# Kernel tuning notes

Measured on AMD Instinct MI355X. Metric: run time of the kernel, lower is better.

Reference implementation:

```python
import jax, jax.numpy as jnp
import numpy as np

D_MODEL, D_HEAD, D_MLP, N_HEADS = 768, 64, 3072, 12
BATCH, SEQ = 1, 4096
LN_EPS = 1e-05
IGNORE = -100000.0


def setup_inputs() -> dict:
    key = jax.random.key(0)
    ks = jax.random.split(key, 8)
    s = 0.02
    return {
        "resid_pre": jax.random.normal(ks[0], (BATCH, SEQ, D_MODEL), jnp.float32),
        "ln1_w": jnp.ones((D_MODEL,), jnp.float32),
        "ln1_b": jnp.zeros((D_MODEL,), jnp.float32),
        "ln2_w": jnp.ones((D_MODEL,), jnp.float32),
        "ln2_b": jnp.zeros((D_MODEL,), jnp.float32),
        "W_Q": jax.random.normal(ks[1], (N_HEADS, D_MODEL, D_HEAD), jnp.float32) * s,
        "W_K": jax.random.normal(ks[2], (N_HEADS, D_MODEL, D_HEAD), jnp.float32) * s,
        "W_V": jax.random.normal(ks[3], (N_HEADS, D_MODEL, D_HEAD), jnp.float32) * s,
        "W_O": jax.random.normal(ks[4], (N_HEADS, D_HEAD, D_MODEL), jnp.float32) * s,
        "b_Q": jnp.zeros((N_HEADS, D_HEAD), jnp.float32),
        "b_K": jnp.zeros((N_HEADS, D_HEAD), jnp.float32),
        "b_V": jnp.zeros((N_HEADS, D_HEAD), jnp.float32),
        "b_O": jnp.zeros((D_MODEL,), jnp.float32),
        "W_in": jax.random.normal(ks[5], (D_MODEL, D_MLP), jnp.float32) * s,
        "b_in": jnp.zeros((D_MLP,), jnp.float32),
        "W_out": jax.random.normal(ks[6], (D_MLP, D_MODEL), jnp.float32) * s,
        "b_out": jnp.zeros((D_MODEL,), jnp.float32),
    }


def _layernorm(x, w, b):
    mean = jnp.mean(x, axis=-1, keepdims=True)
    var = jnp.var(x, axis=-1, keepdims=True)  # unbiased=False
    return (x - mean) * jax.lax.rsqrt(var + LN_EPS) * w + b


def _attention(x, W_Q, W_K, W_V, W_O, b_Q, b_K, b_V, b_O):
    # x: [b, s, d_model]; W_{Q,K,V}: [h, d_model, d_head]
    q = jnp.einsum("bsm,hmd->bshd", x, W_Q) + b_Q
    k = jnp.einsum("bsm,hmd->bshd", x, W_K) + b_K
    v = jnp.einsum("bsm,hmd->bshd", x, W_V) + b_V
    scores = jnp.einsum("bqhd,bkhd->bhqk", q, k) / np.sqrt(D_HEAD).astype(np.float32)
    seq = x.shape[1]
    causal = jnp.tril(jnp.ones((seq, seq), bool))  # True where allowed
    scores = jnp.where(causal, scores, IGNORE)
    pattern = jax.nn.softmax(scores, axis=-1)
    z = jnp.einsum("bkhd,bhqk->bqhd", v, pattern)
    return jnp.einsum("bqhd,hdm->bqm", z, W_O) + b_O


def reference(resid_pre, ln1_w, ln1_b, ln2_w, ln2_b,
              W_Q, W_K, W_V, W_O, b_Q, b_K, b_V, b_O,
              W_in, b_in, W_out, b_out):
    resid_mid = _attention(_layernorm(resid_pre, ln1_w, ln1_b),
                           W_Q, W_K, W_V, W_O, b_Q, b_K, b_V, b_O) + resid_pre
    pre = jnp.einsum("bsm,mf->bsf", _layernorm(resid_mid, ln2_w, ln2_b), W_in) + b_in
    post = jax.nn.gelu(pre, approximate=False)  # torch F.gelu default = exact erf
    mlp_out = jnp.einsum("bsf,fm->bsm", post, W_out) + b_out
    resid_post = mlp_out + resid_mid
    return (resid_post, post)
```

## Files before the change

kernel.cpp:

```cpp
#include <hip/hip_runtime.h>
#include <hip/hip_bf16.h>
#include <math.h>

using bf16 = __hip_bfloat16;
using u16  = unsigned short;
using u32  = unsigned int;
using short8 = __attribute__((ext_vector_type(8))) short;
using f32x4  = __attribute__((ext_vector_type(4))) float;

#define AS1 __attribute__((address_space(1)))
#define AS3 __attribute__((address_space(3)))

__device__ __forceinline__ void gld_lds16(const void* g, void* l) {
  __builtin_amdgcn_global_load_lds((const AS1 u32*)g, (AS3 u32*)l, 16, 0, 0);
}

__device__ __forceinline__ bool probe_f32(const void* p) {
  return *(const u32*)p == 0x3F800000u;
}
__device__ __forceinline__ float ldf(const void* p, size_t i, bool f32) {
  return f32 ? ((const float*)p)[i] : __bfloat162float(((const bf16*)p)[i]);
}
__device__ __forceinline__ void stf(void* p, size_t i, float v, bool f32) {
  if (f32) ((float*)p)[i] = v;
  else     ((bf16*)p)[i] = __float2bfloat16(v);
}
__device__ __forceinline__ u32 cvt_pk_bf16(float lo, float hi) {
  u32 r;
  asm("v_cvt_pk_bf16_f32 %0, %1, %2" : "=v"(r) : "v"(lo), "v"(hi));
  return r;
}

__global__ __launch_bounds__(256) void ln_kernel(const void* __restrict__ x,
    const void* __restrict__ w, const void* __restrict__ b, bf16* __restrict__ out,
    const void* probe, int x_is_f32)
{
  const bool pf = probe_f32(probe);
  const bool xf = x_is_f32 ? true : pf;
  const int row = blockIdx.x, t = threadIdx.x;
  const size_t base = (size_t)row * 768;
  float v[3]; float s1 = 0.f, s2 = 0.f;
#pragma unroll
  for (int i = 0; i < 3; ++i) { float f = ldf(x, base + i*256 + t, xf); v[i] = f; s1 += f; s2 += f*f; }
#pragma unroll
  for (int off = 32; off >= 1; off >>= 1) { s1 += __shfl_xor(s1, off); s2 += __shfl_xor(s2, off); }
  __shared__ float a1[4], a2[4];
  if ((t & 63) == 0) { a1[t>>6] = s1; a2[t>>6] = s2; }
  __syncthreads();
  float S1 = a1[0]+a1[1]+a1[2]+a1[3];
  float S2 = a2[0]+a2[1]+a2[2]+a2[3];
  float mean = S1 * (1.f/768.f);
  float var  = S2 * (1.f/768.f) - mean*mean;
  float rs = rsqrtf(var + 1e-5f);
#pragma unroll
  for (int i = 0; i < 3; ++i) {
    int c = i*256 + t;
    out[base + c] = __float2bfloat16((v[i]-mean)*rs*ldf(w, c, pf) + ldf(b, c, pf));
  }
}

__global__ __launch_bounds__(256) void prep_all(
    const void* W_Q, const void* W_K, const void* W_V, const void* Wo,
    const void* Win, const void* Wout,
    const void* bQ, const void* bK, const void* bV, const void* bO,
    const void* bIn, const void* bOut,
    bf16* __restrict__ qkvT, bf16* __restrict__ WoT, bf16* __restrict__ WinT,
    bf16* __restrict__ WoutT, float* __restrict__ biasA,
    const void* __restrict__ xres, const void* lw, const void* lb,
    bf16* __restrict__ lnout, const void* probe)
{
  const bool pf = probe_f32(probe);
  const int bid = blockIdx.x;
  const int t = threadIdx.x;
  if (bid >= 6939) {
    const int row = bid - 6939;
    const size_t base = (size_t)row * 768;
    float v[3]; float s1 = 0.f, s2 = 0.f;
#pragma unroll
    for (int i = 0; i < 3; ++i) { float f = ldf(xres, base + i*256 + t, pf); v[i] = f; s1 += f; s2 += f*f; }
#pragma unroll
    for (int off = 32; off >= 1; off >>= 1) { s1 += __shfl_xor(s1, off); s2 += __shfl_xor(s2, off); }
    __shared__ float a1[4], a2[4];
    if ((t & 63) == 0) { a1[t>>6] = s1; a2[t>>6] = s2; }
    __syncthreads();
    float S1 = a1[0]+a1[1]+a1[2]+a1[3];
    float S2 = a2[0]+a2[1]+a2[2]+a2[3];
    float mean = S1 * (1.f/768.f);
    float var  = S2 * (1.f/768.f) - mean*mean;
    float rs = rsqrtf(var + 1e-5f);
#pragma unroll
    for (int i = 0; i < 3; ++i) {
      int c = i*256 + t;
      lnout[base + c] = __float2bfloat16((v[i]-mean)*rs*ldf(lw, c, pf) + ldf(lb, c, pf));
    }
    return;
  }
  if (bid >= 6912) {
    int i = (bid - 6912)*256 + t;
    float v;
    if (i < 2304)      v = (i < 768) ? ldf(bQ, i, pf) : (i < 1536 ? ldf(bK, i-768, pf) : ldf(bV, i-1536, pf));
    else if (i < 3072) v = ldf(bO, i-2304, pf);
    else if (i < 6144) v = ldf(bIn, i-3072, pf);
    else               v = ldf(bOut, i-6144, pf);
    biasA[i] = v;
    return;
  }
  const void* src; bf16* dst; int R, C, bx, by; size_t soff = 0;
  if (bid < 1728) {
    int mtx = bid / 576, within = bid % 576;
    int h = within / 48, tt = within % 48;
    by = tt >> 1; bx = tt & 1;
    src = (mtx == 0) ? W_Q : (mtx == 1 ? W_K : W_V);
    soff = (size_t)h * 49152;
    dst = qkvT + ((size_t)mtx*768 + h*64) * 768;
    R = 768; C = 64;
  } else if (bid < 2304) {
    int within = bid - 1728; bx = within % 24; by = within / 24;
    src = Wo; dst = WoT; R = 768; C = 768;
  } else if (bid < 4608) {
    int within = bid - 2304; bx = within % 96; by = within / 96;
    src = Win; dst = WinT; R = 768; C = 3072;
  } else {
    int within = bid - 4608; bx = within % 24; by = within / 24;
    src = Wout; dst = WoutT; R = 3072; C = 768;
  }
  __shared__ bf16 tile[32][33];
  const int bc = bx*32, br = by*32;
  const int tx = t & 31, ty = t >> 5;
#pragma unroll
  for (int i = 0; i < 32; i += 8)
    tile[ty+i][tx] = __float2bfloat16(ldf(src, soff + (size_t)(br+ty+i)*C + bc + tx, pf));
  __syncthreads();
#pragma unroll
  for (int i = 0; i < 32; i += 8)
    dst[(size_t)(bc+ty+i)*R + br + tx] = tile[tx][ty+i];
}

template<int MODE, int BM, int BN, int BK>
__global__ __launch_bounds__(256) void gemm_bt(const bf16* __restrict__ A,
    const bf16* __restrict__ BT, const float* __restrict__ bias,
    const void* __restrict__ res, void* __restrict__ Cout, bf16* __restrict__ aux,
    size_t outOff, const void* probe, int M, int N, int K,
    float* __restrict__ zf, float* __restrict__ sf)
{
  constexpr int MR = BM/32, NR = BN/32;
  constexpr int CH = BK/8;
  __shared__ bf16 Alds[2][BM*BK];
  __shared__ bf16 Blds[2][BN*BK];
  const int tid = threadIdx.x;
  const int lane = tid & 63, w = tid >> 6;
  const int l15 = lane & 15, l4 = lane >> 4;

  const int nwg = gridDim.x * gridDim.y;
  const int L = blockIdx.x + blockIdx.y * gridDim.x;
  const int wid = (L & 7) * (nwg >> 3) + (L >> 3);
  const int bx = wid % gridDim.x, by = wid / gridDim.x;

  if (MODE == 0) {
    float4 z4 = {0.f, 0.f, 0.f, 0.f};
    float4* zp = (float4*)zf + (size_t)wid*1024;
#pragma unroll
    for (int i = 0; i < 4; ++i) zp[i*256 + tid] = z4;
    if (tid < 16) ((float4*)sf)[wid*16 + tid] = z4;
  }

  const int brow = by * BM, bcol = bx * BN;
  const int wr = (w >> 1) * (BM/2), wc = (w & 1) * (BN/2);
  const bf16* Ag = A  + (size_t)brow * K;
  const bf16* Bg = BT + (size_t)bcol * K;
  f32x4 acc[MR][NR];
#pragma unroll
  for (int i = 0; i < MR; ++i)
#pragma unroll
    for (int j = 0; j < NR; ++j) acc[i][j] = 0.f;

  auto swzf = [](int r) { return BK == 64 ? ((r ^ (r >> 3)) & 7) : ((r >> 1) & 3); };

  auto STAGE = [&](int bb, int kt) {
    if (MODE == 4) {
      const float* Zfp = (const float*)A;
      const float* sfh = sf + (size_t)(kt >> 6) * 4096 + brow;
#pragma unroll
      for (int i = 0; i < BM*CH/256; ++i) {
        int id = i*256 + tid, r = id >> 3, cc = id & 7;
        int sw = swzf(r);
        const float* srcp = Zfp + (size_t)(brow + r)*768 + kt + cc*8;
        float4 f0 = *(const float4*)srcp;
        float4 f1 = *(const float4*)(srcp + 4);
        float sc = __builtin_amdgcn_rcpf(sfh[r]);
        u32 pk[4];
        pk[0] = cvt_pk_bf16(f0.x*sc, f0.y*sc);
        pk[1] = cvt_pk_bf16(f0.z*sc, f0.w*sc);
        pk[2] = cvt_pk_bf16(f1.x*sc, f1.y*sc);
        pk[3] = cvt_pk_bf16(f1.z*sc, f1.w*sc);
        *(uint4*)((char*)Alds[bb] + r*(BK*2) + ((cc ^ sw) << 4)) = *(uint4*)pk;
      }
    } else {
#pragma unroll
      for (int i = 0; i < (BM*CH + 255)/256; ++i) {
        int id = i*256 + tid;
        if ((BM*CH % 256) == 0 || id < BM*CH) {
          int r = id / CH, cc = id % CH;
          gld_lds16(Ag + (size_t)r*K + kt + ((cc ^ swzf(r)) * 8), (char*)Alds[bb] + id*16);
        }
      }
    }
#pragma unroll
    for (int i = 0; i < (BN*CH + 255)/256; ++i) {
      int id = i*256 + tid;
      if ((BN*CH % 256) == 0 || id < BN*CH) {
        int r = id / CH, cc = id % CH;
        gld_lds16(Bg + (size_t)r*K + kt + ((cc ^ swzf(r)) * 8), (char*)Blds[bb] + id*16);
      }
    }
  };

  STAGE(0, 0);
  __syncthreads();

  const int nIt = K / BK;
  for (int it = 0; it < nIt; ++it) {
    const int cur = it & 1;
    if (it + 1 < nIt) STAGE(cur ^ 1, (it + 1) * BK);
#pragma unroll
    for (int kk = 0; kk < BK/32; ++kk) {
      short8 a[MR], b[NR];
#pragma unroll
      for (int mi = 0; mi < MR; ++mi) {
        int row = wr + mi*16 + l15;
        a[mi] = *(const short8*)((const char*)Alds[cur] + row*(BK*2) + (((kk*4 + l4) ^ swzf(row)) << 4));
      }
#pragma unroll
      for (int ni = 0; ni < NR; ++ni) {
        int row = wc + ni*16 + l15;
        b[ni] = *(const short8*)((const char*)Blds[cur] + row*(BK*2) + (((kk*4 + l4) ^ swzf(row)) << 4));
      }
      __builtin_amdgcn_s_setprio(1);
#pragma unroll
      for (int mi = 0; mi < MR; ++mi)
#pragma unroll
        for (int ni = 0; ni < NR; ++ni)
          acc[mi][ni] = __builtin_amdgcn_mfma_f32_16x16x32_bf16(a[mi], b[ni], acc[mi][ni], 0, 0, 0);
      __builtin_amdgcn_s_setprio(0);
    }
    __syncthreads();
  }

  const bool pf = probe_f32(probe);
#pragma unroll
  for (int mi = 0; mi < MR; ++mi) {
#pragma unroll
    for (int r = 0; r < 4; ++r) {
      int row = brow + wr + mi*16 + l4*4 + r;
      size_t rowoff = (size_t)row * N;
#pragma unroll
      for (int ni = 0; ni < NR; ++ni) {
        int col = bcol + wc + ni*16 + l15;
        float v = acc[mi][ni][r] + bias[col];
        if (MODE == 4) v += ldf(res, rowoff + col, pf);
        if (MODE == 3) v += ((const float*)res)[rowoff + col];
        if (MODE == 2) v = 0.5f * v * (1.0f + erff(v * 0.70710678118654752f));
        if (MODE == 0) ((bf16*)Cout)[rowoff + col] = __float2bfloat16(v);
        else if (MODE == 4) ((float*)Cout)[rowoff + col] = v;
        else {
          stf(Cout, outOff + rowoff + col, v, pf);
          if (MODE == 2) aux[rowoff + col] = __float2bfloat16(v);
        }
      }
    }
  }
}

__global__ __launch_bounds__(256) void attn_kernel(const bf16* __restrict__ QKV,
    float* __restrict__ Zf, float* __restrict__ Sf)
{
  __shared__ bf16 Ks[2][4096];
  __shared__ bf16 VTs[2][4096];
  __shared__ bf16 Ps[4][1024];
  const int L = blockIdx.x + blockIdx.y * 160;
  const int wid = (L & 7) * 240 + (L >> 3);
  const int h = wid / 160;
  const int cid = 159 - (wid % 160);
  int qb, c;
  if (cid < 16)      { qb = cid;                    c = 0; }
  else if (cid < 48) { qb = 16 + ((cid-16) >> 1);   c = (cid-16) & 1; }
  else if (cid < 96) { qb = 32 + (cid-48)/3;        c = (cid-48)%3; }
  else               { qb = 48 + ((cid-96) >> 2);   c = (cid-96) & 3; }
  const int t_lo = c*16, t_hi = min(c*16 + 16, qb + 1);

  const int tid = threadIdx.x, lane = tid & 63, w = tid >> 6;
  const int l15 = lane & 15, l4 = lane >> 4;
  const int q0 = qb * 64;

  short8 qf[2];
#pragma unroll
  for (int kk = 0; kk < 2; ++kk)
    qf[kk] = *(const short8*)(QKV + (size_t)(q0 + w*16 + l15)*2304 + h*64 + kk*32 + l4*8);

  int kaddr[2][4], pst[4], pld[2], vwa[8];
#pragma unroll
  for (int kk = 0; kk < 2; ++kk)
#pragma unroll
    for (int ct = 0; ct < 4; ++ct) {
      int krow = ct*16 + l15, sk = (krow ^ (krow >> 3)) & 7;
      kaddr[kk][ct] = krow*128 + (((kk*4 + l4) ^ sk) << 4);
    }
#pragma unroll
  for (int r = 0; r < 4; ++r) {
    int prow = l4*4 + r, sp = (prow ^ (prow >> 3)) & 7;
    pst[r] = prow*128 + (((l15 >> 1) ^ sp) << 4) + (l15 & 1)*8;
  }
#pragma unroll
  for (int kg = 0; kg < 2; ++kg) {
    int sp2 = (l15 ^ (l15 >> 3)) & 7;
    pld[kg] = l15*128 + (((kg*4 + l4) ^ sp2) << 4);
  }
  const int vw = tid >> 3, vd0 = (tid & 7) * 8;
  const int vk0 = (vw >> 1) + (vw & 1) * 32;
#pragma unroll
  for (int d = 0; d < 8; ++d) {
    int row = vd0 + d, srow = (row ^ (row >> 3)) & 7;
    vwa[d] = row*128 + (((vw >> 2) ^ srow) << 4) + (vw & 3)*4;
  }

  const ptrdiff_t STEP = 64*2304;
  int id0 = tid, r0 = id0 >> 3;
  int s0 = (r0 ^ (r0 >> 3)) & 7, c0 = ((id0 & 7) ^ s0) * 8;
  int id1 = 256 + tid, r1 = id1 >> 3;
  int s1 = (r1 ^ (r1 >> 3)) & 7, c1 = ((id1 & 7) ^ s1) * 8;
  const bf16* kgp0 = QKV + (size_t)(t_lo*64 + r0)*2304 + 768 + h*64 + c0;
  const bf16* kgp1 = QKV + (size_t)(t_lo*64 + r1)*2304 + 768 + h*64 + c1;
  const int ksd0 = id0*16, ksd1 = id1*16;
  const bf16* vgp0 = QKV + (size_t)(t_lo*64 + vk0)*2304 + 1536 + h*64 + vd0;
  const bf16* vgp1 = vgp0 + (size_t)16*2304;
  uint4 va, vb, ka, kb;

  ka = *(const uint4*)kgp0;  kgp0 += STEP;
  kb = *(const uint4*)kgp1;  kgp1 += STEP;
  va = *(const uint4*)vgp0;  vgp0 += STEP;
  vb = *(const uint4*)vgp1;  vgp1 += STEP;
  *(uint4*)((char*)Ks[0] + ksd0) = ka;
  *(uint4*)((char*)Ks[0] + ksd1) = kb;
  {
    const u16* pa = (const u16*)&va; const u16* pb = (const u16*)&vb;
#pragma unroll
    for (int d = 0; d < 8; ++d)
      *(u32*)((char*)VTs[0] + vwa[d]) = (u32)pa[d] | ((u32)pb[d] << 16);
  }
  __syncthreads();

  f32x4 o[4]; f32x4 osum;
#pragma unroll
  for (int dt = 0; dt < 4; ++dt) o[dt] = 0.f;
  osum = 0.f;
  short8 ones8;
#pragma unroll
  for (int j = 0; j < 8; ++j) ones8[j] = 0x3F80;

#define ABODY(CUR, NT) {                                                        \
    const int nt_ = (NT);                                                       \
    const bool pref_ = (nt_ + 1 < t_hi);                                        \
    if (pref_) {                                                                \
      ka = *(const uint4*)kgp0;  kgp0 += STEP;                                  \
      kb = *(const uint4*)kgp1;  kgp1 += STEP;                                  \
      va = *(const uint4*)vgp0;  vgp0 += STEP;                                  \
      vb = *(const uint4*)vgp1;  vgp1 += STEP;                                  \
    }                                                                           \
    f32x4 s4[4];                                                                \
    _Pragma("unroll") for (int ct = 0; ct < 4; ++ct) s4[ct] = 0.f;              \
    __builtin_amdgcn_s_setprio(1);                                              \
    _Pragma("unroll") for (int kk = 0; kk < 2; ++kk)                            \
      _Pragma("unroll") for (int ct = 0; ct < 4; ++ct) {                        \
        short8 bk = *(const short8*)((const char*)Ks[0] + kaddr[kk][ct] + (CUR)*8192); \
        s4[ct] = __builtin_amdgcn_mfma_f32_16x16x32_bf16(qf[kk], bk, s4[ct], 0, 0, 0); \
      }                                                                         \
    __builtin_amdgcn_s_setprio(0);                                              \
    const bool diag_ = (nt_ == qb);                                             \
    _Pragma("unroll") for (int r = 0; r < 4; ++r) {                             \
      float p_[4];                                                              \
      _Pragma("unroll") for (int ct = 0; ct < 4; ++ct) {                        \
        float sv = s4[ct][r] * 0.18033688f;                                     \
        if (diag_ && (ct*16 + l15 > w*16 + l4*4 + r)) sv = -30000.0f;           \
        p_[ct] = exp2f(fminf(sv, 43.0f));                                       \
      }                                                                         \
      uint2 pk;                                                                 \
      pk.x = cvt_pk_bf16(p_[0], p_[1]);                                         \
      pk.y = cvt_pk_bf16(p_[2], p_[3]);                                         \
      *(uint2*)((char*)&Ps[w][0] + pst[r]) = pk;                                \
    }                                                                           \
    __builtin_amdgcn_s_setprio(1);                                              \
    _Pragma("unroll") for (int kg = 0; kg < 2; ++kg) {                          \
      short8 ap = *(const short8*)((const char*)&Ps[w][0] + pld[kg]);           \
      _Pragma("unroll") for (int dt = 0; dt < 4; ++dt) {                        \
        short8 bv = *(const short8*)((const char*)VTs[0] + kaddr[kg][dt] + (CUR)*8192); \
        o[dt] = __builtin_amdgcn_mfma_f32_16x16x32_bf16(ap, bv, o[dt], 0, 0, 0); \
      }                                                                         \
      osum = __builtin_amdgcn_mfma_f32_16x16x32_bf16(ap, ones8, osum, 0, 0, 0); \
    }                                                                           \
    __builtin_amdgcn_s_setprio(0);                                              \
    if (pref_) {                                                                \
      *(uint4*)((char*)Ks[0] + ksd0 + ((CUR)^1)*8192) = ka;                     \
      *(uint4*)((char*)Ks[0] + ksd1 + ((CUR)^1)*8192) = kb;                     \
      const u16* pa_ = (const u16*)&va; const u16* pb_ = (const u16*)&vb;       \
      _Pragma("unroll") for (int d = 0; d < 8; ++d)                             \
        *(u32*)((char*)VTs[0] + vwa[d] + ((CUR)^1)*8192) = (u32)pa_[d] | ((u32)pb_[d] << 16); \
    }                                                                           \
    __syncthreads();                                                            \
  }

  const int n = t_hi - t_lo;
  int j2 = 0;
  for (; j2 + 2 <= n; j2 += 2) {
    ABODY(0, t_lo + j2);
    ABODY(1, t_lo + j2 + 1);
  }
  if (j2 < n) ABODY(0, t_lo + j2);
#undef ABODY

  const int qrow0 = q0 + w*16 + l4*4;
#pragma unroll
  for (int r = 0; r < 4; ++r)
    if (l15 == 0) unsafeAtomicAdd(&Sf[(size_t)h*4096 + qrow0 + r], osum[r]);
#pragma unroll
  for (int dt = 0; dt < 4; ++dt)
#pragma unroll
    for (int r = 0; r < 4; ++r)
      unsafeAtomicAdd(&Zf[(size_t)(qrow0 + r)*768 + h*64 + dt*16 + l15], o[dt][r]);
}

extern "C" void kernel_launch(void* const* d_in, const int* in_sizes, int n_in,
                              void* d_out, int out_size, void* d_ws, size_t ws_size,
                              hipStream_t stream)
{
  (void)in_sizes; (void)n_in; (void)out_size; (void)ws_size;
  const void* resid_pre = d_in[0];
  const void* ln1_w = d_in[1];
  const void* ln1_b = d_in[2];
  const void* ln2_w = d_in[3];
  const void* ln2_b = d_in[4];
  const void* W_Q  = d_in[5];
  const void* W_K  = d_in[6];
  const void* W_V  = d_in[7];
  const void* W_O  = d_in[8];
  const void* b_Q  = d_in[9];
  const void* b_K  = d_in[10];
  const void* b_V  = d_in[11];
  const void* b_O  = d_in[12];
  const void* W_in  = d_in[13];
  const void* b_in  = d_in[14];
  const void* W_out = d_in[15];
  const void* b_out = d_in[16];
  const void* probe = ln1_w;

  char* ws = (char*)d_ws;
  bf16*  qkvT  = (bf16*)(ws + 0);
  bf16*  WoT   = (bf16*)(ws + 3538944);
  bf16*  WinT  = (bf16*)(ws + 4718592);
  bf16*  WoutT = (bf16*)(ws + 9437184);
  float* biasA = (float*)(ws + 14155776);
  bf16*  x1    = (bf16*)(ws + 14183424);
  bf16*  QKV   = (bf16*)(ws + 20474880);
  float* Zf    = (float*)(ws + 39349248);
  float* Sf    = (float*)(ws + 51932160);
  float* mid   = (float*)(ws + 20474880);
  bf16*  x2    = (bf16*)(ws + 58223616);
  bf16*  postB = (bf16*)(ws + 33057792);

  prep_all<<<11035, 256, 0, stream>>>(W_Q, W_K, W_V, W_O, W_in, W_out,
      b_Q, b_K, b_V, b_O, b_in, b_out, qkvT, WoT, WinT, WoutT, biasA,
      resid_pre, ln1_w, ln1_b, x1, probe);

  gemm_bt<0,128,96,32><<<dim3(24,32), 256, 0, stream>>>(x1, qkvT, biasA, nullptr, QKV, nullptr, 0, probe, 4096, 2304, 768, Zf, Sf);
  attn_kernel<<<dim3(160,12), 256, 0, stream>>>(QKV, Zf, Sf);
  gemm_bt<4,64,64,64><<<dim3(12,64), 256, 0, stream>>>((const bf16*)Zf, WoT, biasA+2304, resid_pre, mid, nullptr, 0, probe, 4096, 768, 768, nullptr, Sf);
  ln_kernel<<<4096, 256, 0, stream>>>(mid, ln2_w, ln2_b, x2, probe, 1);
  gemm_bt<2,128,128,32><<<dim3(24,32), 256, 0, stream>>>(x2, WinT, biasA+3072, nullptr, d_out, postB, 3145728, probe, 4096, 3072, 768, nullptr, nullptr);
  gemm_bt<3,64,64,64><<<dim3(12,64), 256, 0, stream>>>(postB, WoutT, biasA+6144, mid, d_out, nullptr, 0, probe, 4096, 768, 3072, nullptr, nullptr);
}
```

Before: 223.8 us.

## Widen attention blocks to 128 query rows with 8 warps and split K/V loading

The attention kernel now uses 512 threads per block covering 128 query rows, so each K/V tile staged in shared memory is reused by twice as many query warps. KV chunks shrink to 8 tiles, and a new triangular work decomposition maps 144 blocks per head. K and V global loads are split between warp halves instead of every thread loading both. The diagonal mask now spans two key tiles per query block. The trade-offs are larger shared memory and block size, which lowers occupancy, and a different load-balance profile.

```diff
diff --git a/kernel.cpp b/kernel.cpp
--- a/kernel.cpp
+++ b/kernel.cpp
@@ -271,33 +271,34 @@
   }
 }
 
-__global__ __launch_bounds__(256) void attn_kernel(const bf16* __restrict__ QKV,
+__global__ __launch_bounds__(512) void attn_kernel(const bf16* __restrict__ QKV,
     float* __restrict__ Zf, float* __restrict__ Sf)
 {
   __shared__ bf16 Ks[2][4096];
   __shared__ bf16 VTs[2][4096];
-  __shared__ bf16 Ps[4][1024];
-  const int L = blockIdx.x + blockIdx.y * 160;
-  const int wid = (L & 7) * 240 + (L >> 3);
-  const int h = wid / 160;
-  const int cid = 159 - (wid % 160);
-  int qb, c;
-  if (cid < 16)      { qb = cid;                    c = 0; }
-  else if (cid < 48) { qb = 16 + ((cid-16) >> 1);   c = (cid-16) & 1; }
-  else if (cid < 96) { qb = 32 + (cid-48)/3;        c = (cid-48)%3; }
-  else               { qb = 48 + ((cid-96) >> 2);   c = (cid-96) & 3; }
-  const int t_lo = c*16, t_hi = min(c*16 + 16, qb + 1);
+  __shared__ bf16 Ps[8][1024];
+  const int L = blockIdx.x + blockIdx.y * 144;
+  const int wid = (L & 7) * 216 + (L >> 3);
+  const int h = wid / 144;
+  const int cid = 143 - (wid % 144);
+  int g = 0;
+  while (cid >= 2*(g+1)*(g+2)) ++g;
+  int loc = cid - 2*g*(g+1);
+  const int qb = 4*g + loc/(g+1);
+  const int c  = loc % (g+1);
+  const int ntiles = 2*qb + 2;
+  const int t_lo = c*8, t_hi = min(t_lo + 8, ntiles);
 
   const int tid = threadIdx.x, lane = tid & 63, w = tid >> 6;
   const int l15 = lane & 15, l4 = lane >> 4;
-  const int q0 = qb * 64;
+  const int q0 = qb * 128;
 
   short8 qf[2];
 #pragma unroll
   for (int kk = 0; kk < 2; ++kk)
     qf[kk] = *(const short8*)(QKV + (size_t)(q0 + w*16 + l15)*2304 + h*64 + kk*32 + l4*8);
 
-  int kaddr[2][4], pst[4], pld[2], vwa[8];
+  int kaddr[2][4], pst[4], pld[2];
 #pragma unroll
   for (int kk = 0; kk < 2; ++kk)
 #pragma unroll
@@ -315,37 +316,41 @@
     int sp2 = (l15 ^ (l15 >> 3)) & 7;
     pld[kg] = l15*128 + (((kg*4 + l4) ^ sp2) << 4);
   }
-  const int vw = tid >> 3, vd0 = (tid & 7) * 8;
+
+  const int st = tid & 255;
+  const int vw = st >> 3, vd0 = (st & 7) * 8;
   const int vk0 = (vw >> 1) + (vw & 1) * 32;
+  int vwa[8];
 #pragma unroll
   for (int d = 0; d < 8; ++d) {
     int row = vd0 + d, srow = (row ^ (row >> 3)) & 7;
     vwa[d] = row*128 + (((vw >> 2) ^ srow) << 4) + (vw & 3)*4;
   }
+  const int id0 = st, r0 = id0 >> 3;
+  const int s0 = (r0 ^ (r0 >> 3)) & 7, c0 = ((id0 & 7) ^ s0) * 8;
+  const int id1 = 256 + st, r1 = id1 >> 3;
+  const int s1 = (r1 ^ (r1 >> 3)) & 7, c1 = ((id1 & 7) ^ s1) * 8;
+  const int ksd0 = id0*16, ksd1 = id1*16;
 
   const ptrdiff_t STEP = 64*2304;
-  int id0 = tid, r0 = id0 >> 3;
-  int s0 = (r0 ^ (r0 >> 3)) & 7, c0 = ((id0 & 7) ^ s0) * 8;
-  int id1 = 256 + tid, r1 = id1 >> 3;
-  int s1 = (r1 ^ (r1 >> 3)) & 7, c1 = ((id1 & 7) ^ s1) * 8;
   const bf16* kgp0 = QKV + (size_t)(t_lo*64 + r0)*2304 + 768 + h*64 + c0;
   const bf16* kgp1 = QKV + (size_t)(t_lo*64 + r1)*2304 + 768 + h*64 + c1;
-  const int ksd0 = id0*16, ksd1 = id1*16;
   const bf16* vgp0 = QKV + (size_t)(t_lo*64 + vk0)*2304 + 1536 + h*64 + vd0;
   const bf16* vgp1 = vgp0 + (size_t)16*2304;
   uint4 va, vb, ka, kb;
 
-  ka = *(const uint4*)kgp0;  kgp0 += STEP;
-  kb = *(const uint4*)kgp1;  kgp1 += STEP;
-  va = *(const uint4*)vgp0;  vgp0 += STEP;
-  vb = *(const uint4*)vgp1;  vgp1 += STEP;
-  *(uint4*)((char*)Ks[0] + ksd0) = ka;
-  *(uint4*)((char*)Ks[0] + ksd1) = kb;
-  {
+  if (w < 4) {
+    va = *(const uint4*)vgp0;  vgp0 += STEP;
+    vb = *(const uint4*)vgp1;  vgp1 += STEP;
     const u16* pa = (const u16*)&va; const u16* pb = (const u16*)&vb;
 #pragma unroll
     for (int d = 0; d < 8; ++d)
       *(u32*)((char*)VTs[0] + vwa[d]) = (u32)pa[d] | ((u32)pb[d] << 16);
+  } else {
+    ka = *(const uint4*)kgp0;  kgp0 += STEP;
+    kb = *(const uint4*)kgp1;  kgp1 += STEP;
+    *(uint4*)((char*)Ks[0] + ksd0) = ka;
+    *(uint4*)((char*)Ks[0] + ksd1) = kb;
   }
   __syncthreads();
 
@@ -361,10 +366,13 @@
     const int nt_ = (NT);                                                       \
     const bool pref_ = (nt_ + 1 < t_hi);                                        \
     if (pref_) {                                                                \
-      ka = *(const uint4*)kgp0;  kgp0 += STEP;                                  \
-      kb = *(const uint4*)kgp1;  kgp1 += STEP;                                  \
-      va = *(const uint4*)vgp0;  vgp0 += STEP;                                  \
-      vb = *(const uint4*)vgp1;  vgp1 += STEP;                                  \
+      if (w < 4) {                                                              \
+        va = *(const uint4*)vgp0;  vgp0 += STEP;                                \
+        vb = *(const uint4*)vgp1;  vgp1 += STEP;                                \
+      } else {                                                                  \
+        ka = *(const uint4*)kgp0;  kgp0 += STEP;                                \
+        kb = *(const uint4*)kgp1;  kgp1 += STEP;                                \
+      }                                                                         \
     }                                                                           \
     f32x4 s4[4];                                                                \
     _Pragma("unroll") for (int ct = 0; ct < 4; ++ct) s4[ct] = 0.f;              \
@@ -375,12 +383,13 @@
         s4[ct] = __builtin_amdgcn_mfma_f32_16x16x32_bf16(qf[kk], bk, s4[ct], 0, 0, 0); \
       }                                                                         \
     __builtin_amdgcn_s_setprio(0);                                              \
-    const bool diag_ = (nt_ == qb);                                             \
+    const int dtile_ = nt_ - 2*qb;                                              \
+    const bool diag_ = (dtile_ >= 0);                                           \
     _Pragma("unroll") for (int r = 0; r < 4; ++r) {                             \
       float p_[4];                                                              \
       _Pragma("unroll") for (int ct = 0; ct < 4; ++ct) {                        \
         float sv = s4[ct][r] * 0.18033688f;                                     \
-        if (diag_ && (ct*16 + l15 > w*16 + l4*4 + r)) sv = -30000.0f;           \
+        if (diag_ && (dtile_*64 + ct*16 + l15 > w*16 + l4*4 + r)) sv = -30000.0f; \
         p_[ct] = exp2f(fminf(sv, 43.0f));                                       \
       }                                                                         \
       uint2 pk;                                                                 \
@@ -399,11 +408,14 @@
     }                                                                           \
     __builtin_amdgcn_s_setprio(0);                                              \
     if (pref_) {                                                                \
-      *(uint4*)((char*)Ks[0] + ksd0 + ((CUR)^1)*8192) = ka;                     \
-      *(uint4*)((char*)Ks[0] + ksd1 + ((CUR)^1)*8192) = kb;                     \
-      const u16* pa_ = (const u16*)&va; const u16* pb_ = (const u16*)&vb;       \
-      _Pragma("unroll") for (int d = 0; d < 8; ++d)                             \
-        *(u32*)((char*)VTs[0] + vwa[d] + ((CUR)^1)*8192) = (u32)pa_[d] | ((u32)pb_[d] << 16); \
+      if (w < 4) {                                                              \
+        const u16* pa_ = (const u16*)&va; const u16* pb_ = (const u16*)&vb;     \
+        _Pragma("unroll") for (int d = 0; d < 8; ++d)                           \
+          *(u32*)((char*)VTs[0] + vwa[d] + ((CUR)^1)*8192) = (u32)pa_[d] | ((u32)pb_[d] << 16); \
+      } else {                                                                  \
+        *(uint4*)((char*)Ks[0] + ksd0 + ((CUR)^1)*8192) = ka;                   \
+        *(uint4*)((char*)Ks[0] + ksd1 + ((CUR)^1)*8192) = kb;                   \
+      }                                                                         \
     }                                                                           \
     __syncthreads();                                                            \
   }
@@ -471,7 +483,7 @@
       resid_pre, ln1_w, ln1_b, x1, probe);
 
   gemm_bt<0,128,96,32><<<dim3(24,32), 256, 0, stream>>>(x1, qkvT, biasA, nullptr, QKV, nullptr, 0, probe, 4096, 2304, 768, Zf, Sf);
-  attn_kernel<<<dim3(160,12), 256, 0, stream>>>(QKV, Zf, Sf);
+  attn_kernel<<<dim3(144,12), 512, 0, stream>>>(QKV, Zf, Sf);
   gemm_bt<4,64,64,64><<<dim3(12,64), 256, 0, stream>>>((const bf16*)Zf, WoT, biasA+2304, resid_pre, mid, nullptr, 0, probe, 4096, 768, 768, nullptr, Sf);
   ln_kernel<<<4096, 256, 0, stream>>>(mid, ln2_w, ln2_b, x2, probe, 1);
   gemm_bt<2,128,128,32><<<dim3(24,32), 256, 0, stream>>>(x2, WinT, biasA+3072, nullptr, d_out, postB, 3145728, probe, 4096, 3072, 768, nullptr, nullptr);
```

Result: slower. 229.4 us (+2.5%).

## Fuse second LayerNorm into out-projection epilogue and MLP-in GEMM prologue

Applied to the files above, without the earlier changes.

Removes the standalone ln_kernel. The attention out-projection GEMM now accumulates per-row sum and sum-of-squares into a workspace buffer with atomics. That buffer is zeroed by the QKV GEMM. The MLP-in GEMM then normalizes the fp32 residual while staging its A tile into LDS, instead of reading a precomputed bf16 x2 through async global-to-LDS loads. This saves a kernel launch and one full write and read of the normalized activations. In exchange the MLP-in GEMM does more work per tile, reads fp32 data, and recomputes the norm for each column tile. Variance from E[x^2]-mean^2 with atomic float sums may also lose some precision.

```diff
diff --git a/kernel.cpp b/kernel.cpp
--- a/kernel.cpp
+++ b/kernel.cpp
@@ -31,49 +31,21 @@
   return r;
 }
 
-__global__ __launch_bounds__(256) void ln_kernel(const void* __restrict__ x,
-    const void* __restrict__ w, const void* __restrict__ b, bf16* __restrict__ out,
-    const void* probe, int x_is_f32)
-{
-  const bool pf = probe_f32(probe);
-  const bool xf = x_is_f32 ? true : pf;
-  const int row = blockIdx.x, t = threadIdx.x;
-  const size_t base = (size_t)row * 768;
-  float v[3]; float s1 = 0.f, s2 = 0.f;
-#pragma unroll
-  for (int i = 0; i < 3; ++i) { float f = ldf(x, base + i*256 + t, xf); v[i] = f; s1 += f; s2 += f*f; }
-#pragma unroll
-  for (int off = 32; off >= 1; off >>= 1) { s1 += __shfl_xor(s1, off); s2 += __shfl_xor(s2, off); }
-  __shared__ float a1[4], a2[4];
-  if ((t & 63) == 0) { a1[t>>6] = s1; a2[t>>6] = s2; }
-  __syncthreads();
-  float S1 = a1[0]+a1[1]+a1[2]+a1[3];
-  float S2 = a2[0]+a2[1]+a2[2]+a2[3];
-  float mean = S1 * (1.f/768.f);
-  float var  = S2 * (1.f/768.f) - mean*mean;
-  float rs = rsqrtf(var + 1e-5f);
-#pragma unroll
-  for (int i = 0; i < 3; ++i) {
-    int c = i*256 + t;
-    out[base + c] = __float2bfloat16((v[i]-mean)*rs*ldf(w, c, pf) + ldf(b, c, pf));
-  }
-}
-
 __global__ __launch_bounds__(256) void prep_all(
     const void* W_Q, const void* W_K, const void* W_V, const void* Wo,
     const void* Win, const void* Wout,
     const void* bQ, const void* bK, const void* bV, const void* bO,
-    const void* bIn, const void* bOut,
+    const void* bIn, const void* bOut, const void* lw2, const void* lb2,
     bf16* __restrict__ qkvT, bf16* __restrict__ WoT, bf16* __restrict__ WinT,
-    bf16* __restrict__ WoutT, float* __restrict__ biasA,
+    bf16* __restrict__ WoutT, float* __restrict__ biasA, float* __restrict__ lnwb,
     const void* __restrict__ xres, const void* lw, const void* lb,
     bf16* __restrict__ lnout, const void* probe)
 {
   const bool pf = probe_f32(probe);
   const int bid = blockIdx.x;
   const int t = threadIdx.x;
-  if (bid >= 6939) {
-    const int row = bid - 6939;
+  if (bid >= 6945) {
+    const int row = bid - 6945;
     const size_t base = (size_t)row * 768;
     float v[3]; float s1 = 0.f, s2 = 0.f;
 #pragma unroll
@@ -97,12 +69,17 @@
   }
   if (bid >= 6912) {
     int i = (bid - 6912)*256 + t;
-    float v;
-    if (i < 2304)      v = (i < 768) ? ldf(bQ, i, pf) : (i < 1536 ? ldf(bK, i-768, pf) : ldf(bV, i-1536, pf));
-    else if (i < 3072) v = ldf(bO, i-2304, pf);
-    else if (i < 6144) v = ldf(bIn, i-3072, pf);
-    else               v = ldf(bOut, i-6144, pf);
-    biasA[i] = v;
+    if (i < 6912) {
+      float v;
+      if (i < 2304)      v = (i < 768) ? ldf(bQ, i, pf) : (i < 1536 ? ldf(bK, i-768, pf) : ldf(bV, i-1536, pf));
+      else if (i < 3072) v = ldf(bO, i-2304, pf);
+      else if (i < 6144) v = ldf(bIn, i-3072, pf);
+      else               v = ldf(bOut, i-6144, pf);
+      biasA[i] = v;
+    } else {
+      int j = i - 6912;
+      lnwb[j] = (j < 768) ? ldf(lw2, j, pf) : ldf(lb2, j-768, pf);
+    }
     return;
   }
   const void* src; bf16* dst; int R, C, bx, by; size_t soff = 0;
@@ -162,6 +139,7 @@
 #pragma unroll
     for (int i = 0; i < 4; ++i) zp[i*256 + tid] = z4;
     if (tid < 16) ((float4*)sf)[wid*16 + tid] = z4;
+    if (wid < 32) ((float*)aux)[wid*256 + tid] = 0.f;
   }
 
   const int brow = by * BM, bcol = bx * BN;
@@ -195,6 +173,28 @@
         pk[3] = cvt_pk_bf16(f1.z*sc, f1.w*sc);
         *(uint4*)((char*)Alds[bb] + r*(BK*2) + ((cc ^ sw) << 4)) = *(uint4*)pk;
       }
+    } else if (MODE == 5) {
+      const float* midp = (const float*)A;
+      const float* lnw = (const float*)res;
+#pragma unroll
+      for (int i = 0; i < BM*CH/256; ++i) {
+        int id = i*256 + tid, r = id >> 2, cc = id & 3;
+        int row = brow + r;
+        float mean = sf[row] * (1.f/768.f);
+        float rstd = rsqrtf(sf[4096 + row] * (1.f/768.f) - mean*mean + 1e-5f);
+        int col = kt + cc*8;
+        const float* sp = midp + (size_t)row*768 + col;
+        float4 f0 = *(const float4*)sp,        f1 = *(const float4*)(sp + 4);
+        float4 w0 = *(const float4*)(lnw + col), w1 = *(const float4*)(lnw + col + 4);
+        float4 b0 = *(const float4*)(lnw + 768 + col), b1 = *(const float4*)(lnw + 768 + col + 4);
+        u32 pk[4];
+        pk[0] = cvt_pk_bf16((f0.x-mean)*rstd*w0.x + b0.x, (f0.y-mean)*rstd*w0.y + b0.y);
+        pk[1] = cvt_pk_bf16((f0.z-mean)*rstd*w0.z + b0.z, (f0.w-mean)*rstd*w0.w + b0.w);
+        pk[2] = cvt_pk_bf16((f1.x-mean)*rstd*w1.x + b1.x, (f1.y-mean)*rstd*w1.y + b1.y);
+        pk[3] = cvt_pk_bf16((f1.z-mean)*rstd*w1.z + b1.z, (f1.w-mean)*rstd*w1.w + b1.w);
+        int sw = swzf(r);
+        *(uint4*)((char*)Alds[bb] + r*(BK*2) + ((cc ^ sw) << 4)) = *(uint4*)pk;
+      }
     } else {
 #pragma unroll
       for (int i = 0; i < (BM*CH + 255)/256; ++i) {
@@ -253,18 +253,32 @@
     for (int r = 0; r < 4; ++r) {
       int row = brow + wr + mi*16 + l4*4 + r;
       size_t rowoff = (size_t)row * N;
+      float rowsum = 0.f, rowsq = 0.f;
 #pragma unroll
       for (int ni = 0; ni < NR; ++ni) {
         int col = bcol + wc + ni*16 + l15;
         float v = acc[mi][ni][r] + bias[col];
         if (MODE == 4) v += ldf(res, rowoff + col, pf);
         if (MODE == 3) v += ((const float*)res)[rowoff + col];
-        if (MODE == 2) v = 0.5f * v * (1.0f + erff(v * 0.70710678118654752f));
+        if (MODE == 5) v = 0.5f * v * (1.0f + erff(v * 0.70710678118654752f));
         if (MODE == 0) ((bf16*)Cout)[rowoff + col] = __float2bfloat16(v);
-        else if (MODE == 4) ((float*)Cout)[rowoff + col] = v;
-        else {
+        else if (MODE == 4) {
+          ((float*)Cout)[rowoff + col] = v;
+          rowsum += v; rowsq += v*v;
+        } else {
           stf(Cout, outOff + rowoff + col, v, pf);
-          if (MODE == 2) aux[rowoff + col] = __float2bfloat16(v);
+          if (MODE == 5) aux[rowoff + col] = __float2bfloat16(v);
+        }
+      }
+      if (MODE == 4) {
+#pragma unroll
+        for (int off = 1; off < 16; off <<= 1) {
+          rowsum += __shfl_xor(rowsum, off);
+          rowsq  += __shfl_xor(rowsq, off);
+        }
+        if (l15 == 0) {
+          unsafeAtomicAdd(&((float*)aux)[row], rowsum);
+          unsafeAtomicAdd(&((float*)aux)[4096 + row], rowsq);
         }
       }
     }
@@ -463,17 +477,17 @@
   float* Zf    = (float*)(ws + 39349248);
   float* Sf    = (float*)(ws + 51932160);
   float* mid   = (float*)(ws + 20474880);
-  bf16*  x2    = (bf16*)(ws + 58223616);
   bf16*  postB = (bf16*)(ws + 33057792);
-
-  prep_all<<<11035, 256, 0, stream>>>(W_Q, W_K, W_V, W_O, W_in, W_out,
-      b_Q, b_K, b_V, b_O, b_in, b_out, qkvT, WoT, WinT, WoutT, biasA,
-      resid_pre, ln1_w, ln1_b, x1, probe);
-
-  gemm_bt<0,128,96,32><<<dim3(24,32), 256, 0, stream>>>(x1, qkvT, biasA, nullptr, QKV, nullptr, 0, probe, 4096, 2304, 768, Zf, Sf);
+  float* Sst   = (float*)(ws + 58223616);
+  float* lnwb  = (float*)(ws + 58256384);
+
+  prep_all<<<11041, 256, 0, stream>>>(W_Q, W_K, W_V, W_O, W_in, W_out,
+      b_Q, b_K, b_V, b_O, b_in, b_out, ln2_w, ln2_b,
+      qkvT, WoT, WinT, WoutT, biasA, lnwb, resid_pre, ln1_w, ln1_b, x1, probe);
+
+  gemm_bt<0,128,96,32><<<dim3(24,32), 256, 0, stream>>>(x1, qkvT, biasA, nullptr, QKV, (bf16*)Sst, 0, probe, 4096, 2304, 768, Zf, Sf);
   attn_kernel<<<dim3(160,12), 256, 0, stream>>>(QKV, Zf, Sf);
-  gemm_bt<4,64,64,64><<<dim3(12,64), 256, 0, stream>>>((const bf16*)Zf, WoT, biasA+2304, resid_pre, mid, nullptr, 0, probe, 4096, 768, 768, nullptr, Sf);
-  ln_kernel<<<4096, 256, 0, stream>>>(mid, ln2_w, ln2_b, x2, probe, 1);
-  gemm_bt<2,128,128,32><<<dim3(24,32), 256, 0, stream>>>(x2, WinT, biasA+3072, nullptr, d_out, postB, 3145728, probe, 4096, 3072, 768, nullptr, nullptr);
+  gemm_bt<4,64,64,64><<<dim3(12,64), 256, 0, stream>>>((const bf16*)Zf, WoT, biasA+2304, resid_pre, mid, (bf16*)Sst, 0, probe, 4096, 768, 768, nullptr, Sf);
+  gemm_bt<5,128,128,32><<<dim3(24,32), 256, 0, stream>>>((const bf16*)mid, WinT, biasA+3072, lnwb, d_out, postB, 3145728, probe, 4096, 3072, 768, nullptr, Sst);
   gemm_bt<3,64,64,64><<<dim3(12,64), 256, 0, stream>>>(postB, WoutT, biasA+6144, mid, d_out, nullptr, 0, probe, 4096, 768, 3072, nullptr, nullptr);
 }
```

Result: slower. 234.4 us (+4.7%).
